# Kernel optimization log

Hardware: AMD Instinct MI355X
Metric: run time of the kernel (lower is better)

The kernel has to match this reference:

```python
import jax, jax.numpy as jnp
import numpy as np

DIM = 768
HEADS = 12
HEAD_DIM = DIM // HEADS
EPS = 1e-5

def setup_inputs() -> dict:
    key = jax.random.key(0)
    ks = jax.random.split(key, 12)
    s = 1.0 / np.sqrt(DIM)
    x = jax.random.normal(ks[0], (4, 2048, DIM), dtype=jnp.float32)
    Wq = jax.random.uniform(ks[1], (DIM, DIM), jnp.float32, -s, s)
    bq = jnp.zeros((DIM,), jnp.float32)
    Wk = jax.random.uniform(ks[2], (DIM, DIM), jnp.float32, -s, s)
    bk = jnp.zeros((DIM,), jnp.float32)
    Wv = jax.random.uniform(ks[3], (DIM, DIM), jnp.float32, -s, s)
    bv = jnp.zeros((DIM,), jnp.float32)
    W1 = jax.random.uniform(ks[4], (DIM, 2 * DIM), jnp.float32, -s, s)
    b1 = jnp.zeros((2 * DIM,), jnp.float32)
    s2 = 1.0 / np.sqrt(2 * DIM)
    W2 = jax.random.uniform(ks[5], (2 * DIM, DIM), jnp.float32, -s2, s2)
    b2 = jnp.zeros((DIM,), jnp.float32)
    gamma = jnp.ones((DIM,), jnp.float32)
    beta = jnp.zeros((DIM,), jnp.float32)
    return {"x": x, "Wq": Wq, "bq": bq, "Wk": Wk, "bk": bk, "Wv": Wv, "bv": bv,
            "W1": W1, "b1": b1, "W2": W2, "b2": b2, "gamma": gamma, "beta": beta}

def reference(x, Wq, bq, Wk, bk, Wv, bv, W1, b1, W2, b2, gamma, beta):
    B, S, _ = x.shape
    # QKV projections -> (B, H, S, Dh)
    q = (x @ Wq + bq).reshape(B, S, HEADS, HEAD_DIM).transpose(0, 2, 1, 3)
    k = (x @ Wk + bk).reshape(B, S, HEADS, HEAD_DIM).transpose(0, 2, 1, 3)
    v = (x @ Wv + bv).reshape(B, S, HEADS, HEAD_DIM).transpose(0, 2, 1, 3)
    scores = jnp.einsum('bhqd,bhkd->bhqk', q, k) / jnp.sqrt(jnp.float32(HEAD_DIM))
    attn = jax.nn.softmax(scores, axis=-1)  # dropout is identity in eval
    ctx = jnp.einsum('bhqk,bhkd->bhqd', attn, v)
    ctx = ctx.transpose(0, 2, 1, 3).reshape(B, S, DIM)
    # MLP
    out = jax.nn.relu(ctx @ W1 + b1) @ W2 + b2
    # residual + LayerNorm
    h = x + out
    mu = jnp.mean(h, axis=-1, keepdims=True)
    var = jnp.mean(jnp.square(h - mu), axis=-1, keepdims=True)
    return (h - mu) * jax.lax.rsqrt(var + EPS) * gamma + beta
```

## Files before the change

### kernel.cpp

```cpp
#include <hip/hip_runtime.h>
#include <stdint.h>

#define DIM 768
#define HDIM 64
#define NHEADS 12
#define SEQ 2048
#define BATCH 4
#define NTOK (BATCH*SEQ)
#define FF 1536
#define QSCALE 0.1803368801111204f

typedef __bf16 bf16x8 __attribute__((ext_vector_type(8)));
typedef float f32x4 __attribute__((ext_vector_type(4)));
typedef unsigned short u16;
typedef unsigned int u32;

static __device__ __forceinline__ u16 f2bf(float f) {
  u32 u = __float_as_uint(f);
  u32 r = (u + 0x7fffu + ((u >> 16) & 1u)) >> 16;
  return (u16)r;
}

static __device__ __forceinline__ void async16(const void* g, void* l) {
  __builtin_amdgcn_global_load_lds(
      (const __attribute__((address_space(1))) u32*)g,
      (__attribute__((address_space(3))) u32*)l, 16, 0, 0);
}


__global__ void conv_bf16(const float* __restrict__ in, u16* __restrict__ out, int n) {
  int i = (blockIdx.x * 256 + threadIdx.x) * 4;
  if (i < n) {
    float4 f = *(const float4*)(in + i);
    uint2 o;
    o.x = (u32)f2bf(f.x) | ((u32)f2bf(f.y) << 16);
    o.y = (u32)f2bf(f.z) | ((u32)f2bf(f.w) << 16);
    *(uint2*)(out + i) = o;
  }
}

__global__ void transp_bf16(const float* __restrict__ W, u16* __restrict__ Wt, int K, int N) {
  __shared__ float tile[32][33];
  const int k0 = blockIdx.x * 32, n0 = blockIdx.y * 32;
  const int tx = threadIdx.x & 31, ty = threadIdx.x >> 5;
#pragma unroll
  for (int i = 0; i < 4; i++)
    tile[ty + 8 * i][tx] = W[(size_t)(k0 + ty + 8 * i) * N + n0 + tx];
  __syncthreads();
#pragma unroll
  for (int i = 0; i < 4; i++)
    Wt[(size_t)(n0 + ty + 8 * i) * K + k0 + tx] = f2bf(tile[tx][ty + 8 * i]);
}

__global__ void concat_bias(const float* __restrict__ a, const float* __restrict__ b,
                            const float* __restrict__ c, float* __restrict__ o) {
  int i = blockIdx.x * 256 + threadIdx.x;
  if (i < DIM) o[i] = a[i];
  else if (i < 2 * DIM) o[i] = b[i - DIM];
  else if (i < 3 * DIM) o[i] = c[i - 2 * DIM];
}


template<int MODE>
__launch_bounds__(256, 2)
__global__ void gemm128(const u16* __restrict__ A, const u16* __restrict__ Bt,
                        const float* __restrict__ bias, void* __restrict__ outp,
                        int K) {
  __shared__ u16 sA[128 * 64];
  __shared__ u16 sB[128 * 64];
  const int t = threadIdx.x;
  const int w = t >> 6;
  const int lane = t & 63;
  const int quad = lane >> 4;
  const int l15 = lane & 15;
  const int m0 = blockIdx.x * 128;
  const int n0 = blockIdx.y * 128;
  const int wr = (w & 1) * 64;
  const int wc = (w >> 1) * 64;

  f32x4 acc[4][4];
#pragma unroll
  for (int i = 0; i < 4; i++)
#pragma unroll
    for (int j = 0; j < 4; j++) acc[i][j] = (f32x4){0.f, 0.f, 0.f, 0.f};

  const int rowA = lane >> 3;
  const int colSw = ((lane & 7) ^ rowA) * 8;

  for (int k0 = 0; k0 < K; k0 += 64) {
    __syncthreads();
#pragma unroll
    for (int j = 0; j < 4; j++) {
      int r0 = (j * 4 + w) * 8;
      async16(A + (size_t)(m0 + r0 + rowA) * K + k0 + colSw, sA + r0 * 64);
      async16(Bt + (size_t)(n0 + r0 + rowA) * K + k0 + colSw, sB + r0 * 64);
    }
    __builtin_amdgcn_s_waitcnt(0);
    __syncthreads();
#pragma unroll
    for (int ks = 0; ks < 64; ks += 32) {
      bf16x8 a[4], b[4];
#pragma unroll
      for (int i = 0; i < 4; i++)
        a[i] = *(const bf16x8*)(sA + (wr + i * 16 + l15) * 64 +
                                ((((ks >> 3) + quad) ^ (l15 & 7)) * 8));
#pragma unroll
      for (int j = 0; j < 4; j++)
        b[j] = *(const bf16x8*)(sB + (wc + j * 16 + l15) * 64 +
                                ((((ks >> 3) + quad) ^ (l15 & 7)) * 8));
#pragma unroll
      for (int i = 0; i < 4; i++)
#pragma unroll
        for (int j = 0; j < 4; j++)
          acc[i][j] = __builtin_amdgcn_mfma_f32_16x16x32_bf16(a[i], b[j], acc[i][j], 0, 0, 0);
    }
  }

#pragma unroll
  for (int i = 0; i < 4; i++) {
#pragma unroll
    for (int j = 0; j < 4; j++) {
#pragma unroll
      for (int r = 0; r < 4; r++) {
        int m = m0 + wr + i * 16 + quad * 4 + r;
        int n = n0 + wc + j * 16 + l15;
        float v = acc[i][j][r] + bias[n];
        if (MODE == 5) {
          int b = m >> 11, s = m & 2047;
          u16* o = (u16*)outp;
          if (n < DIM) {
            int h = n >> 6, d = n & 63;
            o[(((size_t)(b * NHEADS + h) * SEQ + s) << 6) + d] = f2bf(v * QSCALE);
          } else if (n < 2 * DIM) {
            int nn = n - DIM, h = nn >> 6, d = nn & 63;
            o[(size_t)NTOK * DIM + (((size_t)(b * NHEADS + h) * SEQ + s) << 6) + d] = f2bf(v);
          } else {
            int nn = n - 2 * DIM, h = nn >> 6, d = nn & 63;
            o[2 * (size_t)NTOK * DIM + ((size_t)(b * NHEADS + h) * HDIM + d) * SEQ + s] = f2bf(v);
          }
        } else if (MODE == 3) {
          ((u16*)outp)[(size_t)m * FF + n] = f2bf(fmaxf(v, 0.f));
        } else {
          ((float*)outp)[(size_t)m * DIM + n] = v;
        }
      }
    }
  }
}


__launch_bounds__(256, 2)
__global__ void attn(const u16* __restrict__ Q, const u16* __restrict__ Kb,
                     const u16* __restrict__ Vt, u16* __restrict__ Ctx) {
  __shared__ u16 sK[128 * 64];
  __shared__ u16 sV[64 * 128];
  __shared__ u16 sP[4][16 * 128];
  const int t = threadIdx.x, w = t >> 6, lane = t & 63;
  const int quad = lane >> 4, l15 = lane & 15;
  const int qtile = blockIdx.x;
  const int bh = blockIdx.y;
  const size_t qkbase = (size_t)bh * SEQ * HDIM;
  const int q0 = qtile * 64 + w * 16;

  bf16x8 qf[2];
#pragma unroll
  for (int ks = 0; ks < 2; ks++)
    qf[ks] = *(const bf16x8*)(Q + qkbase + (size_t)(q0 + l15) * HDIM + ks * 32 + quad * 8);

  f32x4 o[4];
#pragma unroll
  for (int i = 0; i < 4; i++) o[i] = (f32x4){0.f, 0.f, 0.f, 0.f};
  float rs[4] = {0.f, 0.f, 0.f, 0.f};

  const int rowK = lane >> 3;
  const int colKsw = ((lane & 7) ^ rowK) * 8;
  const int rowVl = lane >> 4;
  const int chV = lane & 15;

  for (int kt = 0; kt < SEQ / 128; kt++) {
    __syncthreads();
#pragma unroll
    for (int j = 0; j < 4; j++) {
      int rk = (j * 4 + w) * 8;
      async16(Kb + qkbase + (size_t)(kt * 128 + rk + rowK) * HDIM + colKsw, sK + rk * 64);
      int rv = (j * 4 + w) * 4;
      int rV = rv + rowVl;
      int cV = (chV ^ (rV & 15)) * 8;
      async16(Vt + qkbase + (size_t)rV * SEQ + kt * 128 + cV, sV + rv * 128);
    }
    __builtin_amdgcn_s_waitcnt(0);
    __syncthreads();

    f32x4 sc[8];
#pragma unroll
    for (int ni = 0; ni < 8; ni++) {
      f32x4 c = (f32x4){0.f, 0.f, 0.f, 0.f};
      bf16x8 b0 = *(const bf16x8*)(sK + (ni * 16 + l15) * 64 + ((quad ^ (l15 & 7)) * 8));
      bf16x8 b1 = *(const bf16x8*)(sK + (ni * 16 + l15) * 64 + (((4 + quad) ^ (l15 & 7)) * 8));
      c = __builtin_amdgcn_mfma_f32_16x16x32_bf16(qf[0], b0, c, 0, 0, 0);
      c = __builtin_amdgcn_mfma_f32_16x16x32_bf16(qf[1], b1, c, 0, 0, 0);
      sc[ni] = c;
    }

    u16* pw = sP[w];
#pragma unroll
    for (int r = 0; r < 4; r++) {
      int prow = quad * 4 + r;
      u16* prb = pw + prow * 128 + (l15 & 7);
      int hi = l15 >> 3;
#pragma unroll
      for (int ni = 0; ni < 8; ni++) {
        float p = __builtin_amdgcn_exp2f(sc[ni][r]);
        rs[r] += p;
        prb[(((ni * 2 + hi) ^ prow) * 8)] = (u16)((__float_as_uint(p) + 0x8000u) >> 16);
      }
    }

#pragma unroll
    for (int ks = 0; ks < 4; ks++) {
      bf16x8 a = *(const bf16x8*)(pw + l15 * 128 + (((ks * 4 + quad) ^ l15) * 8));
#pragma unroll
      for (int di = 0; di < 4; di++) {
        bf16x8 b = *(const bf16x8*)(sV + (di * 16 + l15) * 128 + (((ks * 4 + quad) ^ l15) * 8));
        o[di] = __builtin_amdgcn_mfma_f32_16x16x32_bf16(a, b, o[di], 0, 0, 0);
      }
    }
  }

  int b = bh / NHEADS, h = bh - b * NHEADS;
#pragma unroll
  for (int r = 0; r < 4; r++) {
    float s = rs[r];
#pragma unroll
    for (int off = 1; off < 16; off <<= 1) s += __shfl_xor(s, off);
    float inv = 1.f / s;
    int sq = q0 + quad * 4 + r;
    size_t base = (size_t)(b * SEQ + sq) * DIM + h * HDIM;
#pragma unroll
    for (int di = 0; di < 4; di++)
      Ctx[base + di * 16 + l15] = f2bf(o[di][r] * inv);
  }
}


__launch_bounds__(256)
__global__ void ln_kernel(const float* __restrict__ x, const float* __restrict__ y,
                          const float* __restrict__ gamma, const float* __restrict__ beta,
                          float* __restrict__ out) {
  const int tok = blockIdx.x;
  const int t = threadIdx.x;
  const int w = t >> 6, lane = t & 63;
  const size_t base = (size_t)tok * DIM;
  float h[3];
#pragma unroll
  for (int i = 0; i < 3; i++) h[i] = x[base + t + i * 256] + y[base + t + i * 256];
  float s = h[0] + h[1] + h[2];
#pragma unroll
  for (int off = 32; off >= 1; off >>= 1) s += __shfl_xor(s, off);
  __shared__ float red[4];
  if (lane == 0) red[w] = s;
  __syncthreads();
  float mu = (red[0] + red[1] + red[2] + red[3]) * (1.f / DIM);
  float v = 0.f;
#pragma unroll
  for (int i = 0; i < 3; i++) { h[i] -= mu; v += h[i] * h[i]; }
#pragma unroll
  for (int off = 32; off >= 1; off >>= 1) v += __shfl_xor(v, off);
  __syncthreads();
  if (lane == 0) red[w] = v;
  __syncthreads();
  float var = (red[0] + red[1] + red[2] + red[3]) * (1.f / DIM);
  float rstd = rsqrtf(var + 1e-5f);
#pragma unroll
  for (int i = 0; i < 3; i++) {
    int c = t + i * 256;
    out[base + c] = h[i] * rstd * gamma[c] + beta[c];
  }
}


extern "C" void kernel_launch(void* const* d_in, const int* in_sizes, int n_in,
                              void* d_out, int out_size, void* d_ws, size_t ws_size,
                              hipStream_t stream) {
  const float* x  = (const float*)d_in[0];
  const float* Wq = (const float*)d_in[1];
  const float* bq = (const float*)d_in[2];
  const float* Wk = (const float*)d_in[3];
  const float* bk = (const float*)d_in[4];
  const float* Wv = (const float*)d_in[5];
  const float* bv = (const float*)d_in[6];
  const float* W1 = (const float*)d_in[7];
  const float* b1 = (const float*)d_in[8];
  const float* W2 = (const float*)d_in[9];
  const float* b2 = (const float*)d_in[10];
  const float* gamma = (const float*)d_in[11];
  const float* beta  = (const float*)d_in[12];

  char* ws = (char*)d_ws;
  u16* xb   = (u16*)ws;           ws += (size_t)NTOK * DIM * 2;
  u16* Wqkvt = (u16*)ws;          ws += (size_t)DIM * DIM * 3 * 2;
  u16* W1t  = (u16*)ws;           ws += (size_t)DIM * FF * 2;
  u16* W2t  = (u16*)ws;           ws += (size_t)DIM * FF * 2;
  float* bqkv = (float*)ws;       ws += (size_t)3 * DIM * 4;
  u16* Qb   = (u16*)ws;           ws += (size_t)NTOK * DIM * 2;
  u16* Kbf  = (u16*)ws;           ws += (size_t)NTOK * DIM * 2;
  u16* Vtb  = (u16*)ws;           ws += (size_t)NTOK * DIM * 2;
  u16* Ctx  = (u16*)ws;           ws += (size_t)NTOK * DIM * 2;
  u16* H1   = (u16*)ws;           ws += (size_t)NTOK * FF * 2;
  float* Y2 = (float*)ws;         ws += (size_t)NTOK * DIM * 4;

  conv_bf16<<<(NTOK * DIM) / 1024, 256, 0, stream>>>(x, xb, NTOK * DIM);
  transp_bf16<<<dim3(DIM / 32, DIM / 32), 256, 0, stream>>>(Wq, Wqkvt, DIM, DIM);
  transp_bf16<<<dim3(DIM / 32, DIM / 32), 256, 0, stream>>>(Wk, Wqkvt + DIM * DIM, DIM, DIM);
  transp_bf16<<<dim3(DIM / 32, DIM / 32), 256, 0, stream>>>(Wv, Wqkvt + 2 * DIM * DIM, DIM, DIM);
  transp_bf16<<<dim3(DIM / 32, FF / 32), 256, 0, stream>>>(W1, W1t, DIM, FF);
  transp_bf16<<<dim3(FF / 32, DIM / 32), 256, 0, stream>>>(W2, W2t, FF, DIM);
  concat_bias<<<9, 256, 0, stream>>>(bq, bk, bv, bqkv);

  gemm128<5><<<dim3(NTOK / 128, 3 * DIM / 128), 256, 0, stream>>>(xb, Wqkvt, bqkv, Qb, DIM);

  attn<<<dim3(SEQ / 64, BATCH * NHEADS), 256, 0, stream>>>(Qb, Kbf, Vtb, Ctx);

  gemm128<3><<<dim3(NTOK / 128, FF / 128), 256, 0, stream>>>(Ctx, W1t, b1, H1, DIM);
  gemm128<4><<<dim3(NTOK / 128, DIM / 128), 256, 0, stream>>>(H1, W2t, b2, Y2, FF);

  ln_kernel<<<NTOK, 256, 0, stream>>>(x, Y2, gamma, beta, (float*)d_out);
}
```

Measured before the change: 330.9 us.

## Split attention P tile in halves, raise occupancy, vectorize LayerNorm, merge QKV transposes

```diff
diff --git a/kernel.cpp b/kernel.cpp
--- a/kernel.cpp
+++ b/kernel.cpp
@@ -52,6 +52,22 @@
     Wt[(size_t)(n0 + ty + 8 * i) * K + k0 + tx] = f2bf(tile[tx][ty + 8 * i]);
 }
 
+__global__ void transp_qkv(const float* __restrict__ Wq, const float* __restrict__ Wk,
+                           const float* __restrict__ Wv, u16* __restrict__ Wt) {
+  __shared__ float tile[32][33];
+  const float* W = blockIdx.z == 0 ? Wq : (blockIdx.z == 1 ? Wk : Wv);
+  u16* dst = Wt + (size_t)blockIdx.z * DIM * DIM;
+  const int k0 = blockIdx.x * 32, n0 = blockIdx.y * 32;
+  const int tx = threadIdx.x & 31, ty = threadIdx.x >> 5;
+#pragma unroll
+  for (int i = 0; i < 4; i++)
+    tile[ty + 8 * i][tx] = W[(size_t)(k0 + ty + 8 * i) * DIM + n0 + tx];
+  __syncthreads();
+#pragma unroll
+  for (int i = 0; i < 4; i++)
+    dst[(size_t)(n0 + ty + 8 * i) * DIM + k0 + tx] = f2bf(tile[tx][ty + 8 * i]);
+}
+
 __global__ void concat_bias(const float* __restrict__ a, const float* __restrict__ b,
                             const float* __restrict__ c, float* __restrict__ o) {
   int i = blockIdx.x * 256 + threadIdx.x;
@@ -62,7 +78,7 @@
 
 
 template<int MODE>
-__launch_bounds__(256, 2)
+__launch_bounds__(256, 3)
 __global__ void gemm128(const u16* __restrict__ A, const u16* __restrict__ Bt,
                         const float* __restrict__ bias, void* __restrict__ outp,
                         int K) {
@@ -149,12 +165,12 @@
 }
 
 
-__launch_bounds__(256, 2)
+__launch_bounds__(256, 4)
 __global__ void attn(const u16* __restrict__ Q, const u16* __restrict__ Kb,
                      const u16* __restrict__ Vt, u16* __restrict__ Ctx) {
   __shared__ u16 sK[128 * 64];
   __shared__ u16 sV[64 * 128];
-  __shared__ u16 sP[4][16 * 128];
+  __shared__ u16 sP[4][16 * 64];
   const int t = threadIdx.x, w = t >> 6, lane = t & 63;
   const int quad = lane >> 4, l15 = lane & 15;
   const int qtile = blockIdx.x;
@@ -176,6 +192,7 @@
   const int colKsw = ((lane & 7) ^ rowK) * 8;
   const int rowVl = lane >> 4;
   const int chV = lane & 15;
+  const int hi = l15 >> 3;
 
   for (int kt = 0; kt < SEQ / 128; kt++) {
     __syncthreads();
@@ -191,38 +208,40 @@
     __builtin_amdgcn_s_waitcnt(0);
     __syncthreads();
 
-    f32x4 sc[8];
-#pragma unroll
-    for (int ni = 0; ni < 8; ni++) {
-      f32x4 c = (f32x4){0.f, 0.f, 0.f, 0.f};
-      bf16x8 b0 = *(const bf16x8*)(sK + (ni * 16 + l15) * 64 + ((quad ^ (l15 & 7)) * 8));
-      bf16x8 b1 = *(const bf16x8*)(sK + (ni * 16 + l15) * 64 + (((4 + quad) ^ (l15 & 7)) * 8));
-      c = __builtin_amdgcn_mfma_f32_16x16x32_bf16(qf[0], b0, c, 0, 0, 0);
-      c = __builtin_amdgcn_mfma_f32_16x16x32_bf16(qf[1], b1, c, 0, 0, 0);
-      sc[ni] = c;
-    }
-
     u16* pw = sP[w];
 #pragma unroll
-    for (int r = 0; r < 4; r++) {
-      int prow = quad * 4 + r;
-      u16* prb = pw + prow * 128 + (l15 & 7);
-      int hi = l15 >> 3;
-#pragma unroll
-      for (int ni = 0; ni < 8; ni++) {
-        float p = __builtin_amdgcn_exp2f(sc[ni][r]);
-        rs[r] += p;
-        prb[(((ni * 2 + hi) ^ prow) * 8)] = (u16)((__float_as_uint(p) + 0x8000u) >> 16);
+    for (int hh = 0; hh < 2; hh++) {
+      f32x4 sc[4];
+#pragma unroll
+      for (int n4 = 0; n4 < 4; n4++) {
+        int ni = hh * 4 + n4;
+        f32x4 c = (f32x4){0.f, 0.f, 0.f, 0.f};
+        bf16x8 b0 = *(const bf16x8*)(sK + (ni * 16 + l15) * 64 + ((quad ^ (l15 & 7)) * 8));
+        bf16x8 b1 = *(const bf16x8*)(sK + (ni * 16 + l15) * 64 + (((4 + quad) ^ (l15 & 7)) * 8));
+        c = __builtin_amdgcn_mfma_f32_16x16x32_bf16(qf[0], b0, c, 0, 0, 0);
+        c = __builtin_amdgcn_mfma_f32_16x16x32_bf16(qf[1], b1, c, 0, 0, 0);
+        sc[n4] = c;
       }
-    }
-
-#pragma unroll
-    for (int ks = 0; ks < 4; ks++) {
-      bf16x8 a = *(const bf16x8*)(pw + l15 * 128 + (((ks * 4 + quad) ^ l15) * 8));
-#pragma unroll
-      for (int di = 0; di < 4; di++) {
-        bf16x8 b = *(const bf16x8*)(sV + (di * 16 + l15) * 128 + (((ks * 4 + quad) ^ l15) * 8));
-        o[di] = __builtin_amdgcn_mfma_f32_16x16x32_bf16(a, b, o[di], 0, 0, 0);
+#pragma unroll
+      for (int r = 0; r < 4; r++) {
+        int prow = quad * 4 + r;
+        u16* prb = pw + prow * 64 + (l15 & 7);
+#pragma unroll
+        for (int n4 = 0; n4 < 4; n4++) {
+          float p = __builtin_amdgcn_exp2f(sc[n4][r]);
+          rs[r] += p;
+          prb[(((n4 * 2 + hi) ^ (prow & 7)) * 8)] = (u16)((__float_as_uint(p) + 0x8000u) >> 16);
+        }
+      }
+#pragma unroll
+      for (int ks = 0; ks < 2; ks++) {
+        bf16x8 a = *(const bf16x8*)(pw + l15 * 64 + (((ks * 4 + quad) ^ (l15 & 7)) * 8));
+#pragma unroll
+        for (int di = 0; di < 4; di++) {
+          bf16x8 b = *(const bf16x8*)(sV + (di * 16 + l15) * 128 +
+                                      (((hh * 8 + ks * 4 + quad) ^ l15) * 8));
+          o[di] = __builtin_amdgcn_mfma_f32_16x16x32_bf16(a, b, o[di], 0, 0, 0);
+        }
       }
     }
   }
@@ -243,38 +262,47 @@
 }
 
 
-__launch_bounds__(256)
+__launch_bounds__(64)
 __global__ void ln_kernel(const float* __restrict__ x, const float* __restrict__ y,
                           const float* __restrict__ gamma, const float* __restrict__ beta,
                           float* __restrict__ out) {
   const int tok = blockIdx.x;
-  const int t = threadIdx.x;
-  const int w = t >> 6, lane = t & 63;
-  const size_t base = (size_t)tok * DIM;
-  float h[3];
-#pragma unroll
-  for (int i = 0; i < 3; i++) h[i] = x[base + t + i * 256] + y[base + t + i * 256];
-  float s = h[0] + h[1] + h[2];
+  const int lane = threadIdx.x;
+  const float4* X = (const float4*)(x + (size_t)tok * DIM);
+  const float4* Y = (const float4*)(y + (size_t)tok * DIM);
+  const float4* G = (const float4*)gamma;
+  const float4* Bt = (const float4*)beta;
+  float4* O = (float4*)(out + (size_t)tok * DIM);
+
+  float4 h[3];
+  float s = 0.f;
+#pragma unroll
+  for (int i = 0; i < 3; i++) {
+    float4 a = X[i * 64 + lane], b = Y[i * 64 + lane];
+    h[i].x = a.x + b.x; h[i].y = a.y + b.y; h[i].z = a.z + b.z; h[i].w = a.w + b.w;
+    s += h[i].x + h[i].y + h[i].z + h[i].w;
+  }
 #pragma unroll
   for (int off = 32; off >= 1; off >>= 1) s += __shfl_xor(s, off);
-  __shared__ float red[4];
-  if (lane == 0) red[w] = s;
-  __syncthreads();
-  float mu = (red[0] + red[1] + red[2] + red[3]) * (1.f / DIM);
+  float mu = s * (1.f / DIM);
   float v = 0.f;
 #pragma unroll
-  for (int i = 0; i < 3; i++) { h[i] -= mu; v += h[i] * h[i]; }
+  for (int i = 0; i < 3; i++) {
+    h[i].x -= mu; h[i].y -= mu; h[i].z -= mu; h[i].w -= mu;
+    v += h[i].x * h[i].x + h[i].y * h[i].y + h[i].z * h[i].z + h[i].w * h[i].w;
+  }
 #pragma unroll
   for (int off = 32; off >= 1; off >>= 1) v += __shfl_xor(v, off);
-  __syncthreads();
-  if (lane == 0) red[w] = v;
-  __syncthreads();
-  float var = (red[0] + red[1] + red[2] + red[3]) * (1.f / DIM);
-  float rstd = rsqrtf(var + 1e-5f);
+  float rstd = rsqrtf(v * (1.f / DIM) + 1e-5f);
 #pragma unroll
   for (int i = 0; i < 3; i++) {
-    int c = t + i * 256;
-    out[base + c] = h[i] * rstd * gamma[c] + beta[c];
+    float4 g = G[i * 64 + lane], bt = Bt[i * 64 + lane];
+    float4 r;
+    r.x = h[i].x * rstd * g.x + bt.x;
+    r.y = h[i].y * rstd * g.y + bt.y;
+    r.z = h[i].z * rstd * g.z + bt.z;
+    r.w = h[i].w * rstd * g.w + bt.w;
+    O[i * 64 + lane] = r;
   }
 }
 
@@ -310,9 +338,7 @@
   float* Y2 = (float*)ws;         ws += (size_t)NTOK * DIM * 4;
 
   conv_bf16<<<(NTOK * DIM) / 1024, 256, 0, stream>>>(x, xb, NTOK * DIM);
-  transp_bf16<<<dim3(DIM / 32, DIM / 32), 256, 0, stream>>>(Wq, Wqkvt, DIM, DIM);
-  transp_bf16<<<dim3(DIM / 32, DIM / 32), 256, 0, stream>>>(Wk, Wqkvt + DIM * DIM, DIM, DIM);
-  transp_bf16<<<dim3(DIM / 32, DIM / 32), 256, 0, stream>>>(Wv, Wqkvt + 2 * DIM * DIM, DIM, DIM);
+  transp_qkv<<<dim3(DIM / 32, DIM / 32, 3), 256, 0, stream>>>(Wq, Wk, Wv, Wqkvt);
   transp_bf16<<<dim3(DIM / 32, FF / 32), 256, 0, stream>>>(W1, W1t, DIM, FF);
   transp_bf16<<<dim3(FF / 32, DIM / 32), 256, 0, stream>>>(W2, W2t, FF, DIM);
   concat_bias<<<9, 256, 0, stream>>>(bq, bk, bv, bqkv);
@@ -324,5 +350,5 @@
   gemm128<3><<<dim3(NTOK / 128, FF / 128), 256, 0, stream>>>(Ctx, W1t, b1, H1, DIM);
   gemm128<4><<<dim3(NTOK / 128, DIM / 128), 256, 0, stream>>>(H1, W2t, b2, Y2, FF);
 
-  ln_kernel<<<NTOK, 256, 0, stream>>>(x, Y2, gamma, beta, (float*)d_out);
-}
+  ln_kernel<<<NTOK, 64, 0, stream>>>(x, Y2, gamma, beta, (float*)d_out);
+}
```

After: 308.9 us. 1.07x faster.
